# Kernel tuning notes

Measured on AMD Instinct MI355X. Metric: run time of the kernel, lower is better.

Reference implementation:

```python
import jax, jax.numpy as jnp
import numpy as np

EMBED_DIM = 768
NUM_HEADS = 12
HEAD_DIM = EMBED_DIM // NUM_HEADS


def setup_inputs() -> dict:
    key = jax.random.key(0)
    ks = jax.random.split(key, 5)
    B, N, D = 8, 1024, EMBED_DIM
    s = 1.0 / np.sqrt(D)
    return {
        "x": jax.random.normal(ks[0], (B, N, D), dtype=jnp.float32),
        "qkv_w": jax.random.uniform(ks[1], (D, 3 * D), jnp.float32, -s, s),  # [in, out]
        "qkv_b": jax.random.uniform(ks[2], (3 * D,), jnp.float32, -s, s),
        "proj_w": jax.random.uniform(ks[3], (D, D), jnp.float32, -s, s),
        "proj_b": jax.random.uniform(ks[4], (D,), jnp.float32, -s, s),
    }


def reference(x, qkv_w, qkv_b, proj_w, proj_b):
    B, N, D = x.shape
    H, Hd = NUM_HEADS, HEAD_DIM
    qkv = x @ qkv_w + qkv_b                          # [B, N, 3D]
    qkv = qkv.reshape(B, N, 3, H, Hd)
    q, k, v = (jnp.moveaxis(qkv, 2, 0)[i].transpose(0, 2, 1, 3) for i in range(3))  # each [B, H, N, Hd]
    scores = jnp.einsum("bhnd,bhmd->bhnm", q, k) / np.sqrt(Hd).astype(x.dtype)
    attn = jax.nn.softmax(scores, axis=-1)           # dropout rate 0.0 -> identity
    out = jnp.einsum("bhnm,bhmd->bhnd", attn, v)     # [B, H, N, Hd]
    out = out.transpose(0, 2, 1, 3).reshape(B, N, D)
    return out @ proj_w + proj_b
```

## Files before the change

### kernel.cpp

```cpp
#include <hip/hip_runtime.h>
#include <hip/hip_bf16.h>

typedef __attribute__((ext_vector_type(8))) short short8;
typedef __attribute__((ext_vector_type(4))) float f32x4;
typedef __attribute__((ext_vector_type(2))) unsigned int uint2v;
typedef __attribute__((ext_vector_type(4))) unsigned int uint4v;
typedef unsigned int u32;

#define QSCALE 0.1803368801111204f

__device__ inline ushort f2bf(float f) {
    unsigned int i = __builtin_bit_cast(unsigned int, f);
    unsigned int r = (i + 0x7FFFu + ((i >> 16) & 1u)) >> 16;
    return (ushort)r;
}
__device__ inline u32 pack_bf16(float a, float b) {
    float2 f2; f2.x = a; f2.y = b;
    __hip_bfloat162 h = __float22bfloat162_rn(f2);
    u32 r; __builtin_memcpy(&r, &h, 4);
    return r;
}

__device__ __forceinline__ void gload_lds16(const ushort* g, ushort* l) {
    __builtin_amdgcn_global_load_lds(
        (const __attribute__((address_space(1))) u32*)g,
        (__attribute__((address_space(3))) u32*)l, 16, 0, 0);
}

__global__ __launch_bounds__(256) void convert_f32_bf16(
    const float* __restrict__ in, ushort* __restrict__ outp, int n8)
{
    int idx = blockIdx.x * 256 + threadIdx.x;
    if (idx >= n8) return;
    const float4 u0 = *(const float4*)&in[(size_t)idx * 8];
    const float4 u1 = *(const float4*)&in[(size_t)idx * 8 + 4];
    uint2v a, b;
    a.x = pack_bf16(u0.x, u0.y); a.y = pack_bf16(u0.z, u0.w);
    b.x = pack_bf16(u1.x, u1.y); b.y = pack_bf16(u1.z, u1.w);
    *(uint2v*)&outp[(size_t)idx * 8] = a;
    *(uint2v*)&outp[(size_t)idx * 8 + 4] = b;
}

__global__ __launch_bounds__(256) void transpose_f32_bf16(
    const float* __restrict__ W, ushort* __restrict__ Wt, int K, int N)
{
    __shared__ float tile[32][33];
    const int n0 = blockIdx.x * 32;
    const int k0 = blockIdx.y * 32;
    const int tx = threadIdx.x & 31;
    const int ty = threadIdx.x >> 5;
    for (int i = ty; i < 32; i += 8)
        tile[i][tx] = W[(size_t)(k0 + i) * N + n0 + tx];
    __syncthreads();
    for (int i = ty; i < 32; i += 8)
        Wt[(size_t)(n0 + i) * K + k0 + tx] = f2bf(tile[tx][i]);
}

template <bool OUT_FP32, bool QKV_MODE>
__global__ __launch_bounds__(256) void gemm_bt(
    const ushort* __restrict__ A, const ushort* __restrict__ Bt,
    const float* __restrict__ bias, void* __restrict__ C,
    ushort* __restrict__ Vt, int M, int N, int K, int ldc)
{
    __shared__ __attribute__((aligned(16))) ushort As[128][64];
    __shared__ __attribute__((aligned(16))) ushort Bs[128][64];
    const int tid  = threadIdx.x;
    const int lane = tid & 63;
    const int w    = tid >> 6;
    const int wm   = (w >> 1) * 64;
    const int wn   = (w & 1) * 64;
    const int g    = lane >> 4;
    const int t    = lane & 15;
    const int m0   = blockIdx.x * 128;
    const int n0   = blockIdx.y * 128;

    const int lr = lane >> 3;
    const int pc = lane & 7;

    f32x4 acc[4][4];
#pragma unroll
    for (int i = 0; i < 4; i++)
#pragma unroll
        for (int j = 0; j < 4; j++) acc[i][j] = {0.f, 0.f, 0.f, 0.f};

    const int xorc = t & 7;

    for (int k0 = 0; k0 < K; k0 += 64) {
#pragma unroll
        for (int p = 0; p < 4; p++) {
            const int row = w * 32 + p * 8 + lr;
            const int gc  = pc ^ (row & 7);
            gload_lds16(&A[(size_t)(m0 + row) * K + k0 + gc * 8], &As[w * 32 + p * 8][0]);
            gload_lds16(&Bt[(size_t)(n0 + row) * K + k0 + gc * 8], &Bs[w * 32 + p * 8][0]);
        }
        __syncthreads();
#pragma unroll
        for (int s = 0; s < 2; s++) {
            short8 a[4], b[4];
            const int ca = ((s * 4 + g) ^ xorc) * 8;
#pragma unroll
            for (int i = 0; i < 4; i++)
                a[i] = *(const short8*)&As[wm + i * 16 + t][ca];
#pragma unroll
            for (int j = 0; j < 4; j++)
                b[j] = *(const short8*)&Bs[wn + j * 16 + t][ca];
#pragma unroll
            for (int i = 0; i < 4; i++)
#pragma unroll
                for (int j = 0; j < 4; j++)
                    acc[i][j] = __builtin_amdgcn_mfma_f32_16x16x32_bf16(
                        a[i], b[j], acc[i][j], 0, 0, 0);
        }
        __syncthreads();
    }

#pragma unroll
    for (int j = 0; j < 4; j++) {
        int col = n0 + wn + j * 16 + t;
        float bv = bias[col];
        if (QKV_MODE && col >= 1536) {
            int h = (col - 1536) >> 6, d = col & 63;
#pragma unroll
            for (int i = 0; i < 4; i++) {
                int n = m0 + wm + i * 16 + g * 4;
                int bb = n >> 10, nn = n & 1023;
                uint2v u;
                u.x = pack_bf16(acc[i][j][0] + bv, acc[i][j][1] + bv);
                u.y = pack_bf16(acc[i][j][2] + bv, acc[i][j][3] + bv);
                *(uint2v*)&Vt[(((size_t)bb * 12 + h) * 64 + d) * 1024 + nn] = u;
            }
        } else {
#pragma unroll
            for (int i = 0; i < 4; i++)
#pragma unroll
                for (int r = 0; r < 4; r++) {
                    int row = m0 + wm + i * 16 + g * 4 + r;
                    float val = acc[i][j][r] + bv;
                    if (QKV_MODE && col < 768) val *= QSCALE;
                    if (OUT_FP32) ((float*)C)[(size_t)row * ldc + col] = val;
                    else          ((ushort*)C)[(size_t)row * ldc + col] = f2bf(val);
                }
        }
    }
}

__global__ __launch_bounds__(256) void gemm_bt2(
    const ushort* __restrict__ A, const ushort* __restrict__ Bt,
    const float* __restrict__ bias, float* __restrict__ C,
    int M, int N, int K, int ldc)
{
    __shared__ __attribute__((aligned(16))) ushort As[64][64];
    __shared__ __attribute__((aligned(16))) ushort Bs[128][64];
    const int tid  = threadIdx.x;
    const int lane = tid & 63;
    const int w    = tid >> 6;
    const int g    = lane >> 4;
    const int t    = lane & 15;
    const int m0   = blockIdx.x * 64;
    const int n0   = blockIdx.y * 128;
    const int wn   = w * 32;

    const int lr = lane >> 3;
    const int pc = lane & 7;

    f32x4 acc[4][2];
#pragma unroll
    for (int i = 0; i < 4; i++)
#pragma unroll
        for (int j = 0; j < 2; j++) acc[i][j] = {0.f, 0.f, 0.f, 0.f};

    const int xorc = t & 7;

    for (int k0 = 0; k0 < K; k0 += 64) {
#pragma unroll
        for (int p = 0; p < 2; p++) {
            const int row = w * 16 + p * 8 + lr;
            const int gc  = pc ^ (row & 7);
            gload_lds16(&A[(size_t)(m0 + row) * K + k0 + gc * 8], &As[w * 16 + p * 8][0]);
        }
#pragma unroll
        for (int p = 0; p < 4; p++) {
            const int row = w * 32 + p * 8 + lr;
            const int gc  = pc ^ (row & 7);
            gload_lds16(&Bt[(size_t)(n0 + row) * K + k0 + gc * 8], &Bs[w * 32 + p * 8][0]);
        }
        __syncthreads();
#pragma unroll
        for (int s = 0; s < 2; s++) {
            short8 a[4], b[2];
            const int ca = ((s * 4 + g) ^ xorc) * 8;
#pragma unroll
            for (int i = 0; i < 4; i++)
                a[i] = *(const short8*)&As[i * 16 + t][ca];
#pragma unroll
            for (int j = 0; j < 2; j++)
                b[j] = *(const short8*)&Bs[wn + j * 16 + t][ca];
#pragma unroll
            for (int i = 0; i < 4; i++)
#pragma unroll
                for (int j = 0; j < 2; j++)
                    acc[i][j] = __builtin_amdgcn_mfma_f32_16x16x32_bf16(
                        a[i], b[j], acc[i][j], 0, 0, 0);
        }
        __syncthreads();
    }

#pragma unroll
    for (int j = 0; j < 2; j++) {
        int col = n0 + wn + j * 16 + t;
        float bv = bias[col];
#pragma unroll
        for (int i = 0; i < 4; i++)
#pragma unroll
            for (int r = 0; r < 4; r++) {
                int row = m0 + i * 16 + g * 4 + r;
                C[(size_t)row * ldc + col] = acc[i][j][r] + bv;
            }
    }
}

__global__ __launch_bounds__(256) void attn_kernel(
    const ushort* __restrict__ qk, const ushort* __restrict__ Vt,
    ushort* __restrict__ out)
{
    __shared__ __attribute__((aligned(16))) ushort Ks[2][64][64];
    __shared__ __attribute__((aligned(16))) ushort Vs[2][64][64];

    const int tid  = threadIdx.x;
    const int lane = tid & 63;
    const int w    = tid >> 6;
    const int g    = lane >> 4;
    const int t    = lane & 15;
    const int bh   = blockIdx.x;
    const int b    = bh / 12;
    const int h    = bh - b * 12;
    const int q0   = blockIdx.y * 64;

    const int srow = tid >> 3;
    const int pc   = tid & 7;
    const size_t base  = (size_t)b * 1024 * 1536;
    const size_t vbase = ((size_t)b * 12 + h) * 64 * 1024;

    short8 qfrag[2];
#pragma unroll
    for (int s = 0; s < 2; s++)
        qfrag[s] = *(const short8*)&qk[base +
            (size_t)(q0 + w * 16 + t) * 1536 + h * 64 + s * 32 + g * 8];

#pragma unroll
    for (int p = 0; p < 2; p++) {
        int r = srow + 32 * p;
        int c = (pc ^ (r & 7)) * 8;
        *(short8*)&Ks[0][r][c] =
            *(const short8*)&qk[base + (size_t)r * 1536 + 768 + h * 64 + pc * 8];
        *(short8*)&Vs[0][r][c] =
            *(const short8*)&Vt[vbase + (size_t)r * 1024 + pc * 8];
    }
    __syncthreads();

    f32x4 o_acc[4];
#pragma unroll
    for (int j = 0; j < 4; j++) o_acc[j] = {0.f, 0.f, 0.f, 0.f};
    float l_part = 0.f;

    for (int kt = 0; kt < 16; kt++) {
        const int cur = kt & 1;

        short8 kpre[2], vpre[2];
        if (kt < 15) {
            const int kb = (kt + 1) * 64;
#pragma unroll
            for (int p = 0; p < 2; p++) {
                int r = srow + 32 * p;
                kpre[p] = *(const short8*)&qk[base + (size_t)(kb + r) * 1536 + 768 + h * 64 + pc * 8];
                vpre[p] = *(const short8*)&Vt[vbase + (size_t)r * 1024 + kb + pc * 8];
            }
        }

        short8 kf[2][4], bv[2][4];
#pragma unroll
        for (int s = 0; s < 2; s++)
#pragma unroll
            for (int j = 0; j < 4; j++) {
                const int row = j * 16 + t;
                const int c = ((s * 4 + g) ^ (t & 7)) * 8;
                kf[s][j] = *(const short8*)&Ks[cur][row][c];
                bv[s][j] = *(const short8*)&Vs[cur][row][c];
            }

        f32x4 s_acc[4];
#pragma unroll
        for (int j = 0; j < 4; j++) s_acc[j] = {0.f, 0.f, 0.f, 0.f};
        __builtin_amdgcn_s_setprio(1);
#pragma unroll
        for (int s = 0; s < 2; s++)
#pragma unroll
            for (int j = 0; j < 4; j++)
                s_acc[j] = __builtin_amdgcn_mfma_f32_16x16x32_bf16(
                    kf[s][j], qfrag[s], s_acc[j], 0, 0, 0);
        __builtin_amdgcn_s_setprio(0);

        u32 wj[4][2];
#pragma unroll
        for (int j = 0; j < 4; j++) {
            float p0 = __builtin_amdgcn_exp2f(s_acc[j][0]);
            float p1 = __builtin_amdgcn_exp2f(s_acc[j][1]);
            float p2 = __builtin_amdgcn_exp2f(s_acc[j][2]);
            float p3 = __builtin_amdgcn_exp2f(s_acc[j][3]);
            l_part += (p0 + p1) + (p2 + p3);
            wj[j][0] = pack_bf16(p0, p1);
            wj[j][1] = pack_bf16(p2, p3);
        }

        __builtin_amdgcn_s_setprio(1);
#pragma unroll
        for (int s = 0; s < 2; s++) {
            auto r0 = __builtin_amdgcn_permlane32_swap(wj[2 * s][0], wj[2 * s + 1][0], false, false);
            auto r1 = __builtin_amdgcn_permlane32_swap(wj[2 * s][1], wj[2 * s + 1][1], false, false);
            auto m02 = __builtin_amdgcn_permlane16_swap(r0[0], r0[1], false, false);
            auto m13 = __builtin_amdgcn_permlane16_swap(r1[0], r1[1], false, false);
            uint4v av;
            av.x = m02[0];
            av.y = m13[0];
            av.z = m02[1];
            av.w = m13[1];
            short8 a = __builtin_bit_cast(short8, av);
#pragma unroll
            for (int j = 0; j < 4; j++)
                o_acc[j] = __builtin_amdgcn_mfma_f32_16x16x32_bf16(
                    a, bv[s][j], o_acc[j], 0, 0, 0);
        }
        __builtin_amdgcn_s_setprio(0);

        if (kt < 15) {
#pragma unroll
            for (int p = 0; p < 2; p++) {
                int r = srow + 32 * p;
                int c = (pc ^ (r & 7)) * 8;
                *(short8*)&Ks[cur ^ 1][r][c] = kpre[p];
                *(short8*)&Vs[cur ^ 1][r][c] = vpre[p];
            }
        }
        __syncthreads();
    }

    {
        float l_tot = l_part;
        l_tot += __shfl_xor(l_tot, 16);
        l_tot += __shfl_xor(l_tot, 32);
        float il[4];
#pragma unroll
        for (int r = 0; r < 4; r++) il[r] = 1.0f / __shfl(l_tot, g * 4 + r);
#pragma unroll
        for (int r = 0; r < 4; r++) {
            int row = q0 + w * 16 + g * 4 + r;
#pragma unroll
            for (int j = 0; j < 4; j++)
                out[((size_t)(b * 1024 + row)) * 768 + h * 64 + j * 16 + t] =
                    f2bf(o_acc[j][r] * il[r]);
        }
    }
}

extern "C" void kernel_launch(void* const* d_in, const int* in_sizes, int n_in,
                              void* d_out, int out_size, void* d_ws, size_t ws_size,
                              hipStream_t stream)
{
    const float* x      = (const float*)d_in[0];
    const float* qkv_w  = (const float*)d_in[1];
    const float* qkv_b  = (const float*)d_in[2];
    const float* proj_w = (const float*)d_in[3];
    const float* proj_b = (const float*)d_in[4];
    float* out = (float*)d_out;

    char* ws = (char*)d_ws;
    ushort* Wt1 = (ushort*)ws;
    ushort* Wt2 = Wt1 + (size_t)2304 * 768;
    char*   buf = (char*)(Wt2 + (size_t)768 * 768);

    transpose_f32_bf16<<<dim3(72, 24), 256, 0, stream>>>(qkv_w, Wt1, 768, 2304);
    transpose_f32_bf16<<<dim3(24, 24), 256, 0, stream>>>(proj_w, Wt2, 768, 768);

    const size_t wt_bytes   = ((size_t)2304 * 768 + (size_t)768 * 768) * 2;
    const size_t full_bytes = wt_bytes + (size_t)8192 * 768 * 2
                                       + (size_t)8192 * 1536 * 2
                                       + (size_t)8192 * 768 * 2
                                       + (size_t)8192 * 768 * 2;

    if (ws_size >= full_bytes) {
        ushort* xb    = (ushort*)buf;
        ushort* qkO   = xb + (size_t)8192 * 768;
        ushort* VtO   = qkO + (size_t)8192 * 1536;
        ushort* attnO = VtO + (size_t)8192 * 768;
        convert_f32_bf16<<<dim3(3072), 256, 0, stream>>>(x, xb, 786432);
        gemm_bt<false, true><<<dim3(64, 18), 256, 0, stream>>>(
            xb, Wt1, qkv_b, qkO, VtO, 8192, 2304, 768, 1536);
        attn_kernel<<<dim3(96, 16), 256, 0, stream>>>(qkO, VtO, attnO);
        gemm_bt2<<<dim3(128, 6), 256, 0, stream>>>(
            attnO, Wt2, proj_b, out, 8192, 768, 768, 768);
    } else {
        ushort* xbB   = (ushort*)buf;
        ushort* qkB   = xbB + (size_t)1024 * 768;
        ushort* VtB   = qkB + (size_t)1024 * 1536;
        ushort* attnB = VtB + (size_t)1024 * 768;
        for (int b = 0; b < 8; b++) {
            const float* xp = x + (size_t)b * 1024 * 768;
            float* outb = out + (size_t)b * 1024 * 768;
            convert_f32_bf16<<<dim3(384), 256, 0, stream>>>(xp, xbB, 98304);
            gemm_bt<false, true><<<dim3(8, 18), 256, 0, stream>>>(
                xbB, Wt1, qkv_b, qkB, VtB, 1024, 2304, 768, 1536);
            attn_kernel<<<dim3(12, 16), 256, 0, stream>>>(qkB, VtB, attnB);
            gemm_bt2<<<dim3(16, 6), 256, 0, stream>>>(
                attnB, Wt2, proj_b, outb, 1024, 768, 768, 768);
        }
    }
}
```

Measured before the change: 192.5 us.

## Double-buffer LDS tiles in both GEMM kernels to overlap loads with MFMA

Both GEMM kernels get two LDS buffers each for the A and B tiles. The first K-tile is loaded up front, and each later iteration prefetches the next tile into the other buffer while running MFMAs on the current one. One barrier per step remains instead of two. The aim is to hide global-to-LDS load latency behind compute, at the cost of doubling LDS use (64 KB per block in the QKV GEMM), which may lower occupancy.

```diff
diff --git a/kernel.cpp b/kernel.cpp
--- a/kernel.cpp
+++ b/kernel.cpp
@@ -62,8 +62,8 @@
     const float* __restrict__ bias, void* __restrict__ C,
     ushort* __restrict__ Vt, int M, int N, int K, int ldc)
 {
-    __shared__ __attribute__((aligned(16))) ushort As[128][64];
-    __shared__ __attribute__((aligned(16))) ushort Bs[128][64];
+    __shared__ __attribute__((aligned(16))) ushort As[2][128][64];
+    __shared__ __attribute__((aligned(16))) ushort Bs[2][128][64];
     const int tid  = threadIdx.x;
     const int lane = tid & 63;
     const int w    = tid >> 6;
@@ -84,26 +84,39 @@
         for (int j = 0; j < 4; j++) acc[i][j] = {0.f, 0.f, 0.f, 0.f};
 
     const int xorc = t & 7;
-
-    for (int k0 = 0; k0 < K; k0 += 64) {
-#pragma unroll
-        for (int p = 0; p < 4; p++) {
-            const int row = w * 32 + p * 8 + lr;
-            const int gc  = pc ^ (row & 7);
-            gload_lds16(&A[(size_t)(m0 + row) * K + k0 + gc * 8], &As[w * 32 + p * 8][0]);
-            gload_lds16(&Bt[(size_t)(n0 + row) * K + k0 + gc * 8], &Bs[w * 32 + p * 8][0]);
-        }
-        __syncthreads();
+    const int nsteps = K >> 6;
+
+#pragma unroll
+    for (int p = 0; p < 4; p++) {
+        const int row = w * 32 + p * 8 + lr;
+        const int gc  = pc ^ (row & 7);
+        gload_lds16(&A[(size_t)(m0 + row) * K + gc * 8], &As[0][w * 32 + p * 8][0]);
+        gload_lds16(&Bt[(size_t)(n0 + row) * K + gc * 8], &Bs[0][w * 32 + p * 8][0]);
+    }
+    __syncthreads();
+
+    int cur = 0;
+    for (int step = 0; step < nsteps; step++) {
+        if (step + 1 < nsteps) {
+            const int k0 = (step + 1) * 64;
+#pragma unroll
+            for (int p = 0; p < 4; p++) {
+                const int row = w * 32 + p * 8 + lr;
+                const int gc  = pc ^ (row & 7);
+                gload_lds16(&A[(size_t)(m0 + row) * K + k0 + gc * 8], &As[cur ^ 1][w * 32 + p * 8][0]);
+                gload_lds16(&Bt[(size_t)(n0 + row) * K + k0 + gc * 8], &Bs[cur ^ 1][w * 32 + p * 8][0]);
+            }
+        }
 #pragma unroll
         for (int s = 0; s < 2; s++) {
             short8 a[4], b[4];
             const int ca = ((s * 4 + g) ^ xorc) * 8;
 #pragma unroll
             for (int i = 0; i < 4; i++)
-                a[i] = *(const short8*)&As[wm + i * 16 + t][ca];
+                a[i] = *(const short8*)&As[cur][wm + i * 16 + t][ca];
 #pragma unroll
             for (int j = 0; j < 4; j++)
-                b[j] = *(const short8*)&Bs[wn + j * 16 + t][ca];
+                b[j] = *(const short8*)&Bs[cur][wn + j * 16 + t][ca];
 #pragma unroll
             for (int i = 0; i < 4; i++)
 #pragma unroll
@@ -112,6 +125,7 @@
                         a[i], b[j], acc[i][j], 0, 0, 0);
         }
         __syncthreads();
+        cur ^= 1;
     }
 
 #pragma unroll
@@ -149,8 +163,8 @@
     const float* __restrict__ bias, float* __restrict__ C,
     int M, int N, int K, int ldc)
 {
-    __shared__ __attribute__((aligned(16))) ushort As[64][64];
-    __shared__ __attribute__((aligned(16))) ushort Bs[128][64];
+    __shared__ __attribute__((aligned(16))) ushort As[2][64][64];
+    __shared__ __attribute__((aligned(16))) ushort Bs[2][128][64];
     const int tid  = threadIdx.x;
     const int lane = tid & 63;
     const int w    = tid >> 6;
@@ -170,31 +184,49 @@
         for (int j = 0; j < 2; j++) acc[i][j] = {0.f, 0.f, 0.f, 0.f};
 
     const int xorc = t & 7;
-
-    for (int k0 = 0; k0 < K; k0 += 64) {
-#pragma unroll
-        for (int p = 0; p < 2; p++) {
-            const int row = w * 16 + p * 8 + lr;
-            const int gc  = pc ^ (row & 7);
-            gload_lds16(&A[(size_t)(m0 + row) * K + k0 + gc * 8], &As[w * 16 + p * 8][0]);
-        }
-#pragma unroll
-        for (int p = 0; p < 4; p++) {
-            const int row = w * 32 + p * 8 + lr;
-            const int gc  = pc ^ (row & 7);
-            gload_lds16(&Bt[(size_t)(n0 + row) * K + k0 + gc * 8], &Bs[w * 32 + p * 8][0]);
-        }
-        __syncthreads();
+    const int nsteps = K >> 6;
+
+#pragma unroll
+    for (int p = 0; p < 2; p++) {
+        const int row = w * 16 + p * 8 + lr;
+        const int gc  = pc ^ (row & 7);
+        gload_lds16(&A[(size_t)(m0 + row) * K + gc * 8], &As[0][w * 16 + p * 8][0]);
+    }
+#pragma unroll
+    for (int p = 0; p < 4; p++) {
+        const int row = w * 32 + p * 8 + lr;
+        const int gc  = pc ^ (row & 7);
+        gload_lds16(&Bt[(size_t)(n0 + row) * K + gc * 8], &Bs[0][w * 32 + p * 8][0]);
+    }
+    __syncthreads();
+
+    int cur = 0;
+    for (int step = 0; step < nsteps; step++) {
+        if (step + 1 < nsteps) {
+            const int k0 = (step + 1) * 64;
+#pragma unroll
+            for (int p = 0; p < 2; p++) {
+                const int row = w * 16 + p * 8 + lr;
+                const int gc  = pc ^ (row & 7);
+                gload_lds16(&A[(size_t)(m0 + row) * K + k0 + gc * 8], &As[cur ^ 1][w * 16 + p * 8][0]);
+            }
+#pragma unroll
+            for (int p = 0; p < 4; p++) {
+                const int row = w * 32 + p * 8 + lr;
+                const int gc  = pc ^ (row & 7);
+                gload_lds16(&Bt[(size_t)(n0 + row) * K + k0 + gc * 8], &Bs[cur ^ 1][w * 32 + p * 8][0]);
+            }
+        }
 #pragma unroll
         for (int s = 0; s < 2; s++) {
             short8 a[4], b[2];
             const int ca = ((s * 4 + g) ^ xorc) * 8;
 #pragma unroll
             for (int i = 0; i < 4; i++)
-                a[i] = *(const short8*)&As[i * 16 + t][ca];
+                a[i] = *(const short8*)&As[cur][i * 16 + t][ca];
 #pragma unroll
             for (int j = 0; j < 2; j++)
-                b[j] = *(const short8*)&Bs[wn + j * 16 + t][ca];
+                b[j] = *(const short8*)&Bs[cur][wn + j * 16 + t][ca];
 #pragma unroll
             for (int i = 0; i < 4; i++)
 #pragma unroll
@@ -203,6 +235,7 @@
                         a[i], b[j], acc[i][j], 0, 0, 0);
         }
         __syncthreads();
+        cur ^= 1;
     }
 
 #pragma unroll
```

Result: slower. 199.8 us (+3.8%).

## Double-buffer LDS in both GEMM kernels with async prefetch two tiles ahead

Applied to the files above, without the earlier changes.

Both GEMM kernels now keep two LDS buffers. Global-to-LDS loads for tile k+2 are issued right after tile k's fragments are read into registers, so memory latency overlaps with the MFMA work instead of stalling at a barrier each step. Explicit vmcnt/lgkmcnt waits, sched_barriers and setprio around the MFMA block control ordering. In exchange, LDS use doubles (64KB for gemm_bt), which may cut occupancy, and correctness depends on the hand-counted vmcnt values.

```diff
diff --git a/kernel.cpp b/kernel.cpp
--- a/kernel.cpp
+++ b/kernel.cpp
@@ -62,8 +62,8 @@
     const float* __restrict__ bias, void* __restrict__ C,
     ushort* __restrict__ Vt, int M, int N, int K, int ldc)
 {
-    __shared__ __attribute__((aligned(16))) ushort As[128][64];
-    __shared__ __attribute__((aligned(16))) ushort Bs[128][64];
+    __shared__ __attribute__((aligned(16))) ushort As[2][128][64];
+    __shared__ __attribute__((aligned(16))) ushort Bs[2][128][64];
     const int tid  = threadIdx.x;
     const int lane = tid & 63;
     const int w    = tid >> 6;
@@ -76,6 +76,7 @@
 
     const int lr = lane >> 3;
     const int pc = lane & 7;
+    const int xorc = t & 7;
 
     f32x4 acc[4][4];
 #pragma unroll
@@ -83,35 +84,65 @@
 #pragma unroll
         for (int j = 0; j < 4; j++) acc[i][j] = {0.f, 0.f, 0.f, 0.f};
 
-    const int xorc = t & 7;
-
-    for (int k0 = 0; k0 < K; k0 += 64) {
+    const int nsteps = K >> 6;
+
+    auto stage = [&](int buf, int kt) {
+        const int k0 = kt * 64;
 #pragma unroll
         for (int p = 0; p < 4; p++) {
             const int row = w * 32 + p * 8 + lr;
             const int gc  = pc ^ (row & 7);
-            gload_lds16(&A[(size_t)(m0 + row) * K + k0 + gc * 8], &As[w * 32 + p * 8][0]);
-            gload_lds16(&Bt[(size_t)(n0 + row) * K + k0 + gc * 8], &Bs[w * 32 + p * 8][0]);
-        }
-        __syncthreads();
+            gload_lds16(&A[(size_t)(m0 + row) * K + k0 + gc * 8], &As[buf][w * 32 + p * 8][0]);
+            gload_lds16(&Bt[(size_t)(n0 + row) * K + k0 + gc * 8], &Bs[buf][w * 32 + p * 8][0]);
+        }
+    };
+
+    stage(0, 0);
+    stage(1, 1);
+    asm volatile("s_waitcnt vmcnt(8)" ::: "memory");
+    __builtin_amdgcn_sched_barrier(0);
+    __builtin_amdgcn_s_barrier();
+    __builtin_amdgcn_sched_barrier(0);
+
+    for (int kt = 0; kt < nsteps; kt++) {
+        const int cur = kt & 1;
+        short8 a[2][4], b[2][4];
 #pragma unroll
         for (int s = 0; s < 2; s++) {
-            short8 a[4], b[4];
             const int ca = ((s * 4 + g) ^ xorc) * 8;
 #pragma unroll
             for (int i = 0; i < 4; i++)
-                a[i] = *(const short8*)&As[wm + i * 16 + t][ca];
+                a[s][i] = *(const short8*)&As[cur][wm + i * 16 + t][ca];
 #pragma unroll
             for (int j = 0; j < 4; j++)
-                b[j] = *(const short8*)&Bs[wn + j * 16 + t][ca];
+                b[s][j] = *(const short8*)&Bs[cur][wn + j * 16 + t][ca];
+        }
+        asm volatile("s_waitcnt lgkmcnt(0)" ::: "memory");
+        __builtin_amdgcn_sched_barrier(0);
+        __builtin_amdgcn_s_barrier();
+        __builtin_amdgcn_sched_barrier(0);
+        if (kt + 2 < nsteps) stage(cur, kt + 2);
+
+        __builtin_amdgcn_s_setprio(1);
+#pragma unroll
+        for (int s = 0; s < 2; s++)
 #pragma unroll
             for (int i = 0; i < 4; i++)
 #pragma unroll
                 for (int j = 0; j < 4; j++)
                     acc[i][j] = __builtin_amdgcn_mfma_f32_16x16x32_bf16(
-                        a[i], b[j], acc[i][j], 0, 0, 0);
-        }
-        __syncthreads();
+                        a[s][i], b[s][j], acc[i][j], 0, 0, 0);
+        __builtin_amdgcn_s_setprio(0);
+        __builtin_amdgcn_sched_barrier(0);
+
+        if (kt + 2 < nsteps) {
+            asm volatile("s_waitcnt vmcnt(8)" ::: "memory");
+        } else if (kt + 1 < nsteps) {
+            asm volatile("s_waitcnt vmcnt(0)" ::: "memory");
+        }
+        __builtin_amdgcn_sched_barrier(0);
+        if (kt + 1 < nsteps) __builtin_amdgcn_s_barrier();
+        __builtin_amdgcn_sched_barrier(0);
     }
 
 #pragma unroll
@@ -149,8 +180,8 @@
     const float* __restrict__ bias, float* __restrict__ C,
     int M, int N, int K, int ldc)
 {
-    __shared__ __attribute__((aligned(16))) ushort As[64][64];
-    __shared__ __attribute__((aligned(16))) ushort Bs[128][64];
+    __shared__ __attribute__((aligned(16))) ushort As[2][64][64];
+    __shared__ __attribute__((aligned(16))) ushort Bs[2][128][64];
     const int tid  = threadIdx.x;
     const int lane = tid & 63;
     const int w    = tid >> 6;
@@ -162,6 +193,7 @@
 
     const int lr = lane >> 3;
     const int pc = lane & 7;
+    const int xorc = t & 7;
 
     f32x4 acc[4][2];
 #pragma unroll
@@ -169,40 +201,70 @@
 #pragma unroll
         for (int j = 0; j < 2; j++) acc[i][j] = {0.f, 0.f, 0.f, 0.f};
 
-    const int xorc = t & 7;
-
-    for (int k0 = 0; k0 < K; k0 += 64) {
+    const int nsteps = K >> 6;
+
+    auto stage = [&](int buf, int kt) {
+        const int k0 = kt * 64;
 #pragma unroll
         for (int p = 0; p < 2; p++) {
             const int row = w * 16 + p * 8 + lr;
             const int gc  = pc ^ (row & 7);
-            gload_lds16(&A[(size_t)(m0 + row) * K + k0 + gc * 8], &As[w * 16 + p * 8][0]);
+            gload_lds16(&A[(size_t)(m0 + row) * K + k0 + gc * 8], &As[buf][w * 16 + p * 8][0]);
         }
 #pragma unroll
         for (int p = 0; p < 4; p++) {
             const int row = w * 32 + p * 8 + lr;
             const int gc  = pc ^ (row & 7);
-            gload_lds16(&Bt[(size_t)(n0 + row) * K + k0 + gc * 8], &Bs[w * 32 + p * 8][0]);
-        }
-        __syncthreads();
+            gload_lds16(&Bt[(size_t)(n0 + row) * K + k0 + gc * 8], &Bs[buf][w * 32 + p * 8][0]);
+        }
+    };
+
+    stage(0, 0);
+    stage(1, 1);
+    asm volatile("s_waitcnt vmcnt(6)" ::: "memory");
+    __builtin_amdgcn_sched_barrier(0);
+    __builtin_amdgcn_s_barrier();
+    __builtin_amdgcn_sched_barrier(0);
+
+    for (int kt = 0; kt < nsteps; kt++) {
+        const int cur = kt & 1;
+        short8 a[2][4], b[2][2];
 #pragma unroll
         for (int s = 0; s < 2; s++) {
-            short8 a[4], b[2];
             const int ca = ((s * 4 + g) ^ xorc) * 8;
 #pragma unroll
             for (int i = 0; i < 4; i++)
-                a[i] = *(const short8*)&As[i * 16 + t][ca];
+                a[s][i] = *(const short8*)&As[cur][i * 16 + t][ca];
 #pragma unroll
             for (int j = 0; j < 2; j++)
-                b[j] = *(const short8*)&Bs[wn + j * 16 + t][ca];
+                b[s][j] = *(const short8*)&Bs[cur][wn + j * 16 + t][ca];
+        }
+        asm volatile("s_waitcnt lgkmcnt(0)" ::: "memory");
+        __builtin_amdgcn_sched_barrier(0);
+        __builtin_amdgcn_s_barrier();
+        __builtin_amdgcn_sched_barrier(0);
+        if (kt + 2 < nsteps) stage(cur, kt + 2);
+
+        __builtin_amdgcn_s_setprio(1);
+#pragma unroll
+        for (int s = 0; s < 2; s++)
 #pragma unroll
             for (int i = 0; i < 4; i++)
 #pragma unroll
                 for (int j = 0; j < 2; j++)
                     acc[i][j] = __builtin_amdgcn_mfma_f32_16x16x32_bf16(
-                        a[i], b[j], acc[i][j], 0, 0, 0);
-        }
-        __syncthreads();
+                        a[s][i], b[s][j], acc[i][j], 0, 0, 0);
+        __builtin_amdgcn_s_setprio(0);
+        __builtin_amdgcn_sched_barrier(0);
+
+        if (kt + 2 < nsteps) {
+            asm volatile("s_waitcnt vmcnt(6)" ::: "memory");
+        } else if (kt + 1 < nsteps) {
+            asm volatile("s_waitcnt vmcnt(0)" ::: "memory");
+        }
+        __builtin_amdgcn_sched_barrier(0);
+        if (kt + 1 < nsteps) __builtin_amdgcn_s_barrier();
+        __builtin_amdgcn_sched_barrier(0);
     }
 
 #pragma unroll
```

Result: no change. 190.4 us (-1.0%).
